# Kernel optimization log

Measured on AMD Instinct MI355X. Metric: run time of the kernel, lower is better.

The kernel has to match this reference:

```python
import math
import jax, jax.numpy as jnp
import numpy as np

NUM_HEADS = 12


def _key_blocks(x, w):
    # x: [B,S,H,D] -> overlapping key blocks [B, C, 3w, H, D], block c covers
    # original key positions [c*w - w, c*w + 2w) (zero padded at the edges).
    B, S, H, D = x.shape
    C = S // w
    x_pad = jnp.pad(x, ((0, 0), (w, w), (0, 0), (0, 0)))
    idx = (jnp.arange(C) * w)[:, None] + jnp.arange(3 * w)[None, :]  # [C,3w]
    return x_pad[:, idx]


def _band_qk(q, k, w):
    # banded_gemm_qk: scores[b,i,h,j] = q[b,i,h,:] . k[b,i+j-w,h,:], j in [0,2w]
    B, S, H, D = q.shape
    C = S // w
    kb = _key_blocks(k, w)                       # [B,C,3w,H,D]
    qb = q.reshape(B, C, w, H, D)
    s = jnp.einsum('bcxhd,bcyhd->bchxy', qb, kb)  # [B,C,H,w,3w]
    row = jnp.arange(w)[:, None]
    col = row + jnp.arange(2 * w + 1)[None, :]    # diagonal extraction
    band = s[:, :, :, row, col]                   # [B,C,H,w,2w+1]
    return band.transpose(0, 1, 3, 2, 4).reshape(B, S, H, 2 * w + 1)


def _band_pv(p, v, w):
    # banded_gemm_pv: out[b,i,h,:] = sum_j p[b,i,h,j] * v[b,i+j-w,h,:]
    B, S, H, M = p.shape
    C = S // w
    vb = _key_blocks(v, w)                        # [B,C,3w,H,D]
    pb = p.reshape(B, C, w, H, M).transpose(0, 1, 3, 2, 4)  # [B,C,H,w,2w+1]
    row = jnp.arange(w)[:, None]
    col = row + jnp.arange(2 * w + 1)[None, :]
    p_full = jnp.zeros((B, C, H, w, 3 * w), p.dtype).at[:, :, :, row, col].set(pb)
    out = jnp.einsum('bchxy,bcyhd->bcxhd', p_full, vb)  # [B,C,w,H,D]
    return out.reshape(B, S, H, -1)


def setup_inputs():
    key = jax.random.key(0)
    ks = jax.random.split(key, 14)
    B, S, E, G = 2, 4096, 768, 64
    scale = 0.02
    hs = jax.random.normal(ks[0], (B, S, E), jnp.float32)
    mask = jnp.zeros((B, 1, 1, S), jnp.int32).at[:, :, :, :G].set(1)
    def lin(k):
        kw, kb = jax.random.split(k)
        return (jax.random.normal(kw, (E, E), jnp.float32) * scale,
                jax.random.normal(kb, (E,), jnp.float32) * scale)
    Wq, bq = lin(ks[1]); Wk, bk = lin(ks[2]); Wv, bv = lin(ks[3])
    Wqg, bqg = lin(ks[4]); Wkg, bkg = lin(ks[5]); Wvg, bvg = lin(ks[6])
    return dict(hidden_states=hs, attention_mask=mask,
                Wq=Wq, bq=bq, Wk=Wk, bk=bk, Wv=Wv, bv=bv,
                Wqg=Wqg, bqg=bqg, Wkg=Wkg, bkg=bkg, Wvg=Wvg, bvg=bvg,
                window=256, num_global=G)


def reference(hidden_states, attention_mask, Wq, bq, Wk, bk, Wv, bv,
              Wqg, bqg, Wkg, bkg, Wvg, bvg, window, num_global):
    B, S, E = hidden_states.shape
    H = NUM_HEADS
    D = E // H
    w, G = window, num_global
    inv_sqrt_d = 1.0 / math.sqrt(D)

    mask2d = attention_mask.reshape(B, S)
    removed = mask2d != 0  # global (or padding) keys excluded from windowed attn

    q = (hidden_states @ Wq + bq) * inv_sqrt_d
    k = hidden_states @ Wk + bk
    v = hidden_states @ Wv + bv
    q = q.reshape(B, S, H, D)
    k = k.reshape(B, S, H, D)
    v = v.reshape(B, S, H, D)

    # --- local (banded) attention scores ---
    band = _band_qk(q, k, w)                                  # [B,S,H,2w+1]
    key_pos = jnp.arange(S)[:, None] + jnp.arange(-w, w + 1)[None, :]  # [S,2w+1]
    valid = (key_pos >= 0) & (key_pos < S)
    removed_pad = jnp.pad(removed, ((0, 0), (w, w)))
    band_removed = removed_pad[:, key_pos + w]                # [B,S,2w+1]
    keep = valid[None, :, None, :] & (~band_removed)[:, :, None, :]
    band = jnp.where(keep, band, -jnp.inf)

    # --- every-token -> global-token scores (global tokens are first G) ---
    sel = jnp.einsum('blhd,bshd->blhs', q, k[:, :G])          # [B,S,H,G]
    scores = jnp.concatenate([sel, band], axis=-1)            # [B,S,H,G+2w+1]
    probs = jax.nn.softmax(scores.astype(jnp.float32), axis=-1)

    out = jnp.einsum('blhs,bshd->blhd', probs[..., :G], v[:, :G].astype(jnp.float32))
    out = out + _band_pv(probs[..., G:], v.astype(jnp.float32), w)
    out = out.astype(hidden_states.dtype).reshape(B, S, E)

    # --- global tokens attend to everything (separate projections) ---
    hg = hidden_states[:, :G]
    qg = (hg @ Wqg + bqg).reshape(B, G, H, D)
    kg = (hidden_states @ Wkg + bkg).reshape(B, S, H, D)
    vg = (hidden_states @ Wvg + bvg).reshape(B, S, H, D)
    gs = jnp.einsum('bghd,bshd->bhgs', qg, kg) * inv_sqrt_d   # [B,H,G,S]
    gp = jax.nn.softmax(gs.astype(jnp.float32), axis=-1)
    go = jnp.einsum('bhgs,bshd->bghd', gp, vg.astype(jnp.float32)).reshape(B, G, E)
    out = out.at[:, :G].set(go.astype(out.dtype))
    return out
```

## Files before the change

### kernel.cpp

```cpp
#include <hip/hip_runtime.h>
#include <hip/hip_bf16.h>


#define BB 2
#define SS 4096
#define EE 768
#define HH 12
#define DD 64
#define WW 256
#define GG 64
#define NSPLIT 16

typedef unsigned short u16;
typedef __attribute__((ext_vector_type(4))) float f4v;
typedef __attribute__((ext_vector_type(8))) short s8v;
typedef __attribute__((ext_vector_type(4))) int i4v;
typedef __attribute__((ext_vector_type(4))) unsigned short us4v;

#define MFMA_BF16(a, b, c) __builtin_amdgcn_mfma_f32_16x16x32_bf16((a), (b), (c), 0, 0, 0)

constexpr long NSE     = (long)BB * SS * EE;
constexpr long OFF_HSB = 0;
constexpr long OFF_WT  = OFF_HSB + NSE;
constexpr long OFF_Q   = OFF_WT + 6L * EE * EE;
constexpr long OFF_K   = OFF_Q + NSE;
constexpr long OFF_V   = OFF_K + NSE;
constexpr long OFF_KG  = OFF_V + NSE;
constexpr long OFF_VG  = OFF_KG + NSE;
constexpr long OFF_QG  = OFF_VG + NSE;
constexpr long OFF_VT  = OFF_QG + (long)BB * GG * EE;
constexpr long OFF_VGT = OFF_VT + NSE;

constexpr long NQTILE = (long)BB * HH * 4;
constexpr int  NLB    = BB * HH * 63;

__device__ __forceinline__ u16 f2bf(float f) {
  unsigned u = __float_as_uint(f);
  u += 0x7fffu + ((u >> 16) & 1u);
  return (u16)(u >> 16);
}

__device__ __forceinline__ unsigned pk_bf16(float a, float b) {
  union { __hip_bfloat162 h; unsigned u; } c;
  c.h = __float22bfloat162_rn(make_float2(a, b));
  return c.u;
}

__global__ __launch_bounds__(256) void k_prep(const float* __restrict__ hs,
                                              const float* __restrict__ Wq, const float* __restrict__ Wk,
                                              const float* __restrict__ Wv, const float* __restrict__ Wkg,
                                              const float* __restrict__ Wvg, const float* __restrict__ Wqg,
                                              u16* __restrict__ ws) {
  int bid = blockIdx.x;
  if (bid < 6144) {
    long i = ((long)bid * 256 + threadIdx.x) * 4;
    f4v v = *(const f4v*)(hs + i);
    us4v o;
#pragma unroll
    for (int j = 0; j < 4; ++j) o[j] = f2bf(v[j]);
    *(us4v*)(ws + OFF_HSB + i) = o;
    return;
  }
  int wb = bid - 6144;
  int widx = wb / 576; int rem = wb % 576; int kt = rem / 24; int nt = rem % 24;
  const float* src;
  switch (widx) {
    case 0: src = Wq; break; case 1: src = Wk; break; case 2: src = Wv; break;
    case 3: src = Wkg; break; case 4: src = Wvg; break; default: src = Wqg; break;
  }
  __shared__ float tl[32][33];
  int t = threadIdx.x; int r = t >> 3; int c4 = (t & 7) * 4;
  f4v v = *(const f4v*)(src + (long)(kt * 32 + r) * EE + nt * 32 + c4);
#pragma unroll
  for (int j = 0; j < 4; ++j) tl[r][c4 + j] = v[j];
  __syncthreads();
  us4v o;
#pragma unroll
  for (int j = 0; j < 4; ++j) o[j] = f2bf(tl[c4 + j][r]);
  *(us4v*)(ws + OFF_WT + (long)widx * EE * EE + (long)(nt * 32 + r) * EE + kt * 32 + c4) = o;
}

__global__ __launch_bounds__(256, 4) void k_proj(u16* __restrict__ ws,
                                              const float* __restrict__ bq, const float* __restrict__ bk,
                                              const float* __restrict__ bv, const float* __restrict__ bkg,
                                              const float* __restrict__ bvg, const float* __restrict__ bqg) {
  int bid = blockIdx.x;
  int widx, mt, nt;
  if (bid < 1920) {
    int L = (bid & 7) * 240 + (bid >> 3);
    mt = L / 30; int inner = L % 30; widx = inner / 6; nt = inner % 6;
  } else { widx = 5; mt = 0; nt = bid - 1920; }

  __shared__ u16 Al[128 * 64];
  __shared__ u16 Bl[128 * 64];
  int tid = threadIdx.x, lane = tid & 63, wid = tid >> 6;
  int wr = wid >> 1, wc = wid & 1;

  f4v acc[4][4];
#pragma unroll
  for (int i = 0; i < 4; ++i)
#pragma unroll
    for (int j = 0; j < 4; ++j) acc[i][j] = f4v{0.f, 0.f, 0.f, 0.f};

  const u16* hsb = ws + OFF_HSB;
  const u16* Wp  = ws + OFF_WT + (long)widx * EE * EE;

  const u16* asrc[4]; const u16* bsrc[4];
  int dso[4];
#pragma unroll
  for (int it = 0; it < 4; ++it) {
    int c = tid + it * 256;
    int r = c >> 3, j = c & 7;
    long arow;
    if (widx == 5) { int rr = mt * 128 + r; arow = (long)(rr >> 6) * SS + (rr & 63); }
    else           { arow = (long)mt * 128 + r; }
    asrc[it] = hsb + arow * EE + j * 8;
    bsrc[it] = Wp + (long)(nt * 128 + r) * EE + j * 8;
    dso[it]  = r * 64 + (j ^ (r & 7)) * 8;
  }

  const u16* afp[4]; const u16* bfp[4];
#pragma unroll
  for (int f = 0; f < 4; ++f) {
    afp[f] = Al + (wr * 64 + f * 16 + (lane & 15)) * 64;
    bfp[f] = Bl + (wc * 64 + f * 16 + (lane & 15)) * 64;
  }
  int hi4 = lane >> 4, lx = lane & 7;

  i4v areg[4], breg[4];
#pragma unroll
  for (int it = 0; it < 4; ++it) {
    areg[it] = *(const i4v*)(asrc[it]);
    breg[it] = *(const i4v*)(bsrc[it]);
  }
#pragma unroll
  for (int it = 0; it < 4; ++it) {
    *(i4v*)&Al[dso[it]] = areg[it];
    *(i4v*)&Bl[dso[it]] = breg[it];
  }
  __syncthreads();

  for (int t = 0; t < 12; ++t) {
    if (t < 11) {
      int k0n = (t + 1) * 64;
#pragma unroll
      for (int it = 0; it < 4; ++it) {
        areg[it] = *(const i4v*)(asrc[it] + k0n);
        breg[it] = *(const i4v*)(bsrc[it] + k0n);
      }
    }
#pragma unroll
    for (int ks = 0; ks < 2; ++ks) {
      int sw = ((ks * 4 + hi4) ^ lx) * 8;
      s8v af[4], bfr[4];
#pragma unroll
      for (int f = 0; f < 4; ++f) {
        af[f]  = *(const s8v*)(afp[f] + sw);
        bfr[f] = *(const s8v*)(bfp[f] + sw);
      }
#pragma unroll
      for (int i = 0; i < 4; ++i)
#pragma unroll
        for (int j = 0; j < 4; ++j) acc[i][j] = MFMA_BF16(af[i], bfr[j], acc[i][j]);
    }
    __syncthreads();
    if (t < 11) {
#pragma unroll
      for (int it = 0; it < 4; ++it) {
        *(i4v*)&Al[dso[it]] = areg[it];
        *(i4v*)&Bl[dso[it]] = breg[it];
      }
    }
    __syncthreads();
  }

  const float* bias; u16* outp; float scl = 1.0f;
  switch (widx) {
    case 0: bias = bq;  outp = ws + OFF_Q;  scl = 0.125f * 1.44269504f; break;
    case 1: bias = bk;  outp = ws + OFF_K;  break;
    case 2: bias = bv;  outp = ws + OFF_VT;  break;
    case 3: bias = bkg; outp = ws + OFF_KG; break;
    case 4: bias = bvg; outp = ws + OFF_VGT; break;
    default: bias = bqg; outp = ws + OFF_QG; scl = 0.125f * 1.44269504f; break;
  }

  if (widx == 2 || widx == 4) {
    int s0g = mt * 128 + wr * 64 + (lane >> 4) * 4;
#pragma unroll
    for (int fi = 0; fi < 4; ++fi) {
      int srow = s0g + fi * 16;
      int b_ = srow >> 12; int sl = srow & (SS - 1);
#pragma unroll
      for (int fj = 0; fj < 4; ++fj) {
        int col = nt * 128 + wc * 64 + fj * 16 + (lane & 15);
        float bcol = bias[col];
        us4v o;
#pragma unroll
        for (int e = 0; e < 4; ++e) o[e] = f2bf(acc[fi][fj][e] + bcol);
        *(us4v*)&outp[((long)(b_ * HH + (col >> 6)) * DD + (col & 63)) * SS + sl] = o;
      }
    }
  } else {
#pragma unroll
    for (int fi = 0; fi < 4; ++fi)
#pragma unroll
      for (int fj = 0; fj < 4; ++fj) {
        int col = nt * 128 + wc * 64 + fj * 16 + (lane & 15);
        float bcol = bias[col];
#pragma unroll
        for (int e = 0; e < 4; ++e) {
          int rl = wr * 64 + fi * 16 + (lane >> 4) * 4 + e;
          float vv = (acc[fi][fj][e] + bcol) * scl;
          outp[(long)(mt * 128 + rl) * EE + col] = f2bf(vv);
        }
      }
  }
}

__global__ __launch_bounds__(256) void k_lattn(const u16* __restrict__ ws, float* __restrict__ out) {
  int bid0 = blockIdx.x;
  if (bid0 >= NLB) {
    int g = bid0 - NLB;
    int b = g / (HH * 4); int rem = g % (HH * 4); int h = rem >> 2; int qs = rem & 3;
    int tid = threadIdx.x;
    int row = tid >> 4; int c4 = (tid & 15) * 4;

    const float* PA = (const float*)(ws + OFF_V);
    const float* Pm = PA + NQTILE * NSPLIT * 1024L;
    const float* Pl2 = Pm + NQTILE * NSPLIT * 16L;
    long base = (long)g * NSPLIT;

    float M = -1e30f;
#pragma unroll
    for (int s = 0; s < NSPLIT; ++s) M = fmaxf(M, Pm[(base + s) * 16 + row]);
    f4v acc = f4v{0.f, 0.f, 0.f, 0.f};
    float L = 0.f;
#pragma unroll
    for (int s = 0; s < NSPLIT; ++s) {
      float wgt = exp2f(Pm[(base + s) * 16 + row] - M);
      L += wgt * Pl2[(base + s) * 16 + row];
      f4v a = *(const f4v*)&PA[(base + s) * 1024 + row * 64 + c4];
#pragma unroll
      for (int j = 0; j < 4; ++j) acc[j] += wgt * a[j];
    }
    float inv = 1.f / L;
    f4v o;
#pragma unroll
    for (int j = 0; j < 4; ++j) o[j] = acc[j] * inv;
    *(f4v*)&out[((long)b * SS + qs * 16 + row) * EE + h * DD + c4] = o;
    return;
  }

  int bid = (bid0 & 7) * 189 + (bid0 >> 3);
  int b = bid / (HH * 63); int rem = bid % (HH * 63); int h = rem / 63; int qt = rem % 63;
  int l0 = GG + qt * 64;
  int tid = threadIdx.x, lane = tid & 63, wid = tid >> 6;

  __shared__ u16 Kl[64][72];
  __shared__ u16 Vtl[64][72];
  __shared__ u16 Pl[4][16][72];

  const u16* Qp  = ws + OFF_Q + (long)b * SS * EE;
  const u16* Kp  = ws + OFF_K + (long)b * SS * EE;
  const u16* Vtp = ws + OFF_VT + (long)(b * HH + h) * DD * SS;

  int qbase = l0 + wid * 16;
  s8v qf[2];
#pragma unroll
  for (int ks = 0; ks < 2; ++ks)
    qf[ks] = *(const s8v*)(Qp + (long)(qbase + (lane & 15)) * EE + h * DD + ks * 32 + (lane >> 4) * 8);

  float m_r[4], l_p[4]; f4v ao[4];
#pragma unroll
  for (int e = 0; e < 4; ++e) { m_r[e] = -1e30f; l_p[e] = 0.f; }
#pragma unroll
  for (int df = 0; df < 4; ++df) ao[df] = f4v{0.f, 0.f, 0.f, 0.f};

  int lo = (l0 - WW > GG) ? (l0 - WW) : GG;
  int hi = (l0 + 64 + WW < SS) ? (l0 + 64 + WW) : SS;
  int ntile = 1 + ((hi - lo) >> 6);

  const u16* kbase[2]; const u16* vbase[2];
  u16* kdst[2]; u16* vdst[2];
#pragma unroll
  for (int it = 0; it < 2; ++it) {
    int c = tid + it * 256;
    int sr = c >> 3, so = (c & 7) * 8;
    kbase[it] = Kp + (long)sr * EE + h * DD + so;
    vbase[it] = Vtp + (long)sr * SS + so;
    kdst[it] = &Kl[sr][so];
    vdst[it] = &Vtl[sr][so];
  }

  i4v kreg[2], vreg[2];
#pragma unroll
  for (int it = 0; it < 2; ++it) {
    kreg[it] = *(const i4v*)(kbase[it]);
    vreg[it] = *(const i4v*)(vbase[it]);
  }
#pragma unroll
  for (int it = 0; it < 2; ++it) {
    *(i4v*)kdst[it] = kreg[it];
    *(i4v*)vdst[it] = vreg[it];
  }
  __syncthreads();

  for (int t = 0; t < ntile; ++t) {
    int kb = (t == 0) ? 0 : lo + (t - 1) * 64;
    if (t + 1 < ntile) {
      int kbn = lo + t * 64;
#pragma unroll
      for (int it = 0; it < 2; ++it) {
        kreg[it] = *(const i4v*)(kbase[it] + (long)kbn * EE);
        vreg[it] = *(const i4v*)(vbase[it] + kbn);
      }
    }

    f4v sc[4];
#pragma unroll
    for (int c = 0; c < 4; ++c) sc[c] = f4v{0.f, 0.f, 0.f, 0.f};
    __builtin_amdgcn_s_setprio(1);
#pragma unroll
    for (int c = 0; c < 4; ++c)
#pragma unroll
      for (int ks = 0; ks < 2; ++ks) {
        s8v kf = *(const s8v*)&Kl[c * 16 + (lane & 15)][ks * 32 + (lane >> 4) * 8];
        sc[c] = MFMA_BF16(qf[ks], kf, sc[c]);
      }
    __builtin_amdgcn_s_setprio(0);

    if (t > 0 && (kb <= l0 - WW || kb >= l0 + WW)) {
#pragma unroll
      for (int c = 0; c < 4; ++c) {
        int key = kb + c * 16 + (lane & 15);
#pragma unroll
        for (int e = 0; e < 4; ++e) {
          int qrow = qbase + (lane >> 4) * 4 + e;
          if (key < qrow - WW || key > qrow + WW) sc[c][e] = -1e30f;
        }
      }
    }

    float pmax[4];
#pragma unroll
    for (int e = 0; e < 4; ++e)
      pmax[e] = fmaxf(fmaxf(sc[0][e], sc[1][e]), fmaxf(sc[2][e], sc[3][e]));
    bool need;
    if (t == 0) need = true;
    else {
      bool ok = (pmax[0] <= m_r[0] + 11.5f) & (pmax[1] <= m_r[1] + 11.5f) &
                (pmax[2] <= m_r[2] + 11.5f) & (pmax[3] <= m_r[3] + 11.5f);
      need = !__all(ok);
    }
    if (need) {
#pragma unroll
      for (int e = 0; e < 4; ++e) {
        float rm = pmax[e];
#pragma unroll
        for (int off = 1; off < 16; off <<= 1) rm = fmaxf(rm, __shfl_xor(rm, off));
        float mn = fmaxf(m_r[e], rm);
        float scl = exp2f(m_r[e] - mn);
        l_p[e] *= scl;
#pragma unroll
        for (int df = 0; df < 4; ++df) ao[df][e] *= scl;
        m_r[e] = mn;
      }
    }

#pragma unroll
    for (int e = 0; e < 4; ++e) {
      float p0 = exp2f(sc[0][e] - m_r[e]);
      float p1 = exp2f(sc[1][e] - m_r[e]);
      float p2 = exp2f(sc[2][e] - m_r[e]);
      float p3 = exp2f(sc[3][e] - m_r[e]);
      l_p[e] += (p0 + p1) + (p2 + p3);
      unsigned u01 = pk_bf16(p0, p1);
      unsigned u23 = pk_bf16(p2, p3);
      int pr = (lane >> 4) * 4 + e;
      int l15 = lane & 15;
      Pl[wid][pr][l15]      = (u16)u01;
      Pl[wid][pr][16 + l15] = (u16)(u01 >> 16);
      Pl[wid][pr][32 + l15] = (u16)u23;
      Pl[wid][pr][48 + l15] = (u16)(u23 >> 16);
    }

    __builtin_amdgcn_s_setprio(1);
#pragma unroll
    for (int kblk = 0; kblk < 2; ++kblk) {
      s8v pf = *(const s8v*)&Pl[wid][lane & 15][kblk * 32 + (lane >> 4) * 8];
#pragma unroll
      for (int df = 0; df < 4; ++df) {
        s8v vf = *(const s8v*)&Vtl[df * 16 + (lane & 15)][kblk * 32 + (lane >> 4) * 8];
        ao[df] = MFMA_BF16(pf, vf, ao[df]);
      }
    }
    __builtin_amdgcn_s_setprio(0);
    __syncthreads();

    if (t + 1 < ntile) {
#pragma unroll
      for (int it = 0; it < 2; ++it) {
        *(i4v*)kdst[it] = kreg[it];
        *(i4v*)vdst[it] = vreg[it];
      }
    }
    __syncthreads();
  }

  float l_r[4];
#pragma unroll
  for (int e = 0; e < 4; ++e) {
    float s = l_p[e];
#pragma unroll
    for (int off = 1; off < 16; off <<= 1) s += __shfl_xor(s, off);
    l_r[e] = s;
  }
#pragma unroll
  for (int df = 0; df < 4; ++df)
#pragma unroll
    for (int e = 0; e < 4; ++e) {
      int row = qbase + (lane >> 4) * 4 + e;
      int col = h * DD + df * 16 + (lane & 15);
      out[((long)b * SS + row) * EE + col] = ao[df][e] / l_r[e];
    }
}

__global__ __launch_bounds__(64) void k_gattn_part(u16* __restrict__ ws) {
  int bid = blockIdx.x;
  int g = bid / NSPLIT; int sp = bid % NSPLIT;
  int b = g / (HH * 4); int rem = g % (HH * 4); int h = rem >> 2; int qs = rem & 3;
  int lane = threadIdx.x;

  __shared__ u16 Kl[32][72];
  __shared__ u16 Vtl[64][40];
  __shared__ u16 Pl[16][40];

  const u16* Qgp = ws + OFF_QG + (long)b * GG * EE;
  const u16* Kgp = ws + OFF_KG + (long)b * SS * EE;
  const u16* Vtp = ws + OFF_VGT + (long)(b * HH + h) * DD * SS;

  int qbase = qs * 16;
  s8v qf[2];
#pragma unroll
  for (int ks = 0; ks < 2; ++ks)
    qf[ks] = *(const s8v*)(Qgp + (long)(qbase + (lane & 15)) * EE + h * DD + ks * 32 + (lane >> 4) * 8);

  float m_r[4], l_p[4]; f4v ao[4];
#pragma unroll
  for (int e = 0; e < 4; ++e) { m_r[e] = -1e30f; l_p[e] = 0.f; }
#pragma unroll
  for (int df = 0; df < 4; ++df) ao[df] = f4v{0.f, 0.f, 0.f, 0.f};

  int t0 = sp * (SS / 32 / NSPLIT);
  for (int kt = t0; kt < t0 + SS / 32 / NSPLIT; ++kt) {
    int kb = kt * 32;
#pragma unroll
    for (int r2 = 0; r2 < 4; ++r2) {
      int chunk = lane + r2 * 64;
      int kr = chunk >> 3, ko = (chunk & 7) * 8;
      *(i4v*)&Kl[kr][ko] = *(const i4v*)(Kgp + (long)(kb + kr) * EE + h * DD + ko);
      int dr = chunk >> 2, ko2 = (chunk & 3) * 8;
      *(i4v*)&Vtl[dr][ko2] = *(const i4v*)(Vtp + (long)dr * SS + kb + ko2);
    }
    __syncthreads();

    f4v sc[2] = {f4v{0.f, 0.f, 0.f, 0.f}, f4v{0.f, 0.f, 0.f, 0.f}};
#pragma unroll
    for (int c = 0; c < 2; ++c)
#pragma unroll
      for (int ks = 0; ks < 2; ++ks) {
        s8v kf = *(const s8v*)&Kl[c * 16 + (lane & 15)][ks * 32 + (lane >> 4) * 8];
        sc[c] = MFMA_BF16(qf[ks], kf, sc[c]);
      }

    float pmax[4];
#pragma unroll
    for (int e = 0; e < 4; ++e) pmax[e] = fmaxf(sc[0][e], sc[1][e]);
    bool need;
    if (kt == t0) need = true;
    else {
      bool ok = (pmax[0] <= m_r[0] + 11.5f) & (pmax[1] <= m_r[1] + 11.5f) &
                (pmax[2] <= m_r[2] + 11.5f) & (pmax[3] <= m_r[3] + 11.5f);
      need = !__all(ok);
    }
    if (need) {
#pragma unroll
      for (int e = 0; e < 4; ++e) {
        float rm = pmax[e];
#pragma unroll
        for (int off = 1; off < 16; off <<= 1) rm = fmaxf(rm, __shfl_xor(rm, off));
        float mn = fmaxf(m_r[e], rm);
        float scl = exp2f(m_r[e] - mn);
        l_p[e] *= scl;
#pragma unroll
        for (int df = 0; df < 4; ++df) ao[df][e] *= scl;
        m_r[e] = mn;
      }
    }

#pragma unroll
    for (int e = 0; e < 4; ++e) {
      float p0 = exp2f(sc[0][e] - m_r[e]);
      float p1 = exp2f(sc[1][e] - m_r[e]);
      l_p[e] += p0 + p1;
      unsigned u01 = pk_bf16(p0, p1);
      int pr = (lane >> 4) * 4 + e;
      int l15 = lane & 15;
      Pl[pr][l15]      = (u16)u01;
      Pl[pr][16 + l15] = (u16)(u01 >> 16);
    }
    s8v pf = *(const s8v*)&Pl[lane & 15][(lane >> 4) * 8];
#pragma unroll
    for (int df = 0; df < 4; ++df) {
      s8v vf = *(const s8v*)&Vtl[df * 16 + (lane & 15)][(lane >> 4) * 8];
      ao[df] = MFMA_BF16(pf, vf, ao[df]);
    }
    __syncthreads();
  }

  float l_r[4];
#pragma unroll
  for (int e = 0; e < 4; ++e) {
    float s = l_p[e];
#pragma unroll
    for (int off = 1; off < 16; off <<= 1) s += __shfl_xor(s, off);
    l_r[e] = s;
  }

  float* PA = (float*)(ws + OFF_V);
  float* Pm = PA + NQTILE * NSPLIT * 1024L;
  float* Pl2 = Pm + NQTILE * NSPLIT * 16L;
  long pb = (long)g * NSPLIT + sp;
#pragma unroll
  for (int df = 0; df < 4; ++df)
#pragma unroll
    for (int e = 0; e < 4; ++e) {
      int rl = (lane >> 4) * 4 + e;
      PA[pb * 1024 + rl * 64 + df * 16 + (lane & 15)] = ao[df][e];
    }
  if ((lane & 15) == 0) {
#pragma unroll
    for (int e = 0; e < 4; ++e) {
      int rl = (lane >> 4) * 4 + e;
      Pm[pb * 16 + rl] = m_r[e];
      Pl2[pb * 16 + rl] = l_r[e];
    }
  }
}

extern "C" void kernel_launch(void* const* d_in, const int* in_sizes, int n_in,
                              void* d_out, int out_size, void* d_ws, size_t ws_size,
                              hipStream_t stream) {
  const float* hs  = (const float*)d_in[0];
  const float* Wq  = (const float*)d_in[2];  const float* bq  = (const float*)d_in[3];
  const float* Wk  = (const float*)d_in[4];  const float* bk  = (const float*)d_in[5];
  const float* Wv  = (const float*)d_in[6];  const float* bv  = (const float*)d_in[7];
  const float* Wqg = (const float*)d_in[8];  const float* bqg = (const float*)d_in[9];
  const float* Wkg = (const float*)d_in[10]; const float* bkg = (const float*)d_in[11];
  const float* Wvg = (const float*)d_in[12]; const float* bvg = (const float*)d_in[13];
  u16* ws = (u16*)d_ws;
  float* out = (float*)d_out;

  k_prep<<<6144 + 6 * 24 * 24, 256, 0, stream>>>(hs, Wq, Wk, Wv, Wkg, Wvg, Wqg, ws);
  k_proj<<<1926, 256, 0, stream>>>(ws, bq, bk, bv, bkg, bvg, bqg);
  k_gattn_part<<<(int)(NQTILE * NSPLIT), 64, 0, stream>>>(ws);
  k_lattn<<<NLB + (int)NQTILE, 256, 0, stream>>>(ws, out);
}
```

Baseline: 136.0 us.

## Keep P in registers by computing transposed scores and using 16x16x16 MFMA

The local-attention kernel now computes S^T (K as the A operand, Q as B), so each lane holds four consecutive keys for one query row. The probabilities then feed directly as the A operand of a 16x16x16 bf16 MFMA for the PV product. This removes the shared-memory round trip for P and the per-row shuffle reductions; the row max becomes a single value per lane reduced across two shuffles. In exchange it issues twice as many smaller PV MFMAs, adds shuffles to broadcast scale factors to the output layout, and keeps the old path as a fallback when the builtin is missing.

```diff
diff --git a/kernel.cpp b/kernel.cpp
--- a/kernel.cpp
+++ b/kernel.cpp
@@ -14,10 +14,18 @@
 typedef unsigned short u16;
 typedef __attribute__((ext_vector_type(4))) float f4v;
 typedef __attribute__((ext_vector_type(8))) short s8v;
+typedef __attribute__((ext_vector_type(4))) short s4v;
 typedef __attribute__((ext_vector_type(4))) int i4v;
 typedef __attribute__((ext_vector_type(4))) unsigned short us4v;
 
 #define MFMA_BF16(a, b, c) __builtin_amdgcn_mfma_f32_16x16x32_bf16((a), (b), (c), 0, 0, 0)
+
+#if __has_builtin(__builtin_amdgcn_mfma_f32_16x16x16bf16_1k)
+#define HAVE_MFMA16 1
+#define MFMA16(a, b, c) __builtin_amdgcn_mfma_f32_16x16x16bf16_1k((a), (b), (c), 0, 0, 0)
+#else
+#define HAVE_MFMA16 0
+#endif
 
 constexpr long NSE     = (long)BB * SS * EE;
 constexpr long OFF_HSB = 0;
@@ -255,10 +263,13 @@
   int b = bid / (HH * 63); int rem = bid % (HH * 63); int h = rem / 63; int qt = rem % 63;
   int l0 = GG + qt * 64;
   int tid = threadIdx.x, lane = tid & 63, wid = tid >> 6;
+  int l15 = lane & 15, hi4 = lane >> 4;
 
   __shared__ u16 Kl[64][72];
   __shared__ u16 Vtl[64][72];
+#if !HAVE_MFMA16
   __shared__ u16 Pl[4][16][72];
+#endif
 
   const u16* Qp  = ws + OFF_Q + (long)b * SS * EE;
   const u16* Kp  = ws + OFF_K + (long)b * SS * EE;
@@ -268,11 +279,9 @@
   s8v qf[2];
 #pragma unroll
   for (int ks = 0; ks < 2; ++ks)
-    qf[ks] = *(const s8v*)(Qp + (long)(qbase + (lane & 15)) * EE + h * DD + ks * 32 + (lane >> 4) * 8);
-
-  float m_r[4], l_p[4]; f4v ao[4];
-#pragma unroll
-  for (int e = 0; e < 4; ++e) { m_r[e] = -1e30f; l_p[e] = 0.f; }
+    qf[ks] = *(const s8v*)(Qp + (long)(qbase + l15) * EE + h * DD + ks * 32 + hi4 * 8);
+
+  f4v ao[4];
 #pragma unroll
   for (int df = 0; df < 4; ++df) ao[df] = f4v{0.f, 0.f, 0.f, 0.f};
 
@@ -305,6 +314,9 @@
   }
   __syncthreads();
 
+#if HAVE_MFMA16
+  float m_s = -1e30f, l_p = 0.f;
+
   for (int t = 0; t < ntile; ++t) {
     int kb = (t == 0) ? 0 : lo + (t - 1) * 64;
     if (t + 1 < ntile) {
@@ -324,7 +336,123 @@
     for (int c = 0; c < 4; ++c)
 #pragma unroll
       for (int ks = 0; ks < 2; ++ks) {
-        s8v kf = *(const s8v*)&Kl[c * 16 + (lane & 15)][ks * 32 + (lane >> 4) * 8];
+        s8v kf = *(const s8v*)&Kl[c * 16 + l15][ks * 32 + hi4 * 8];
+        sc[c] = MFMA_BF16(kf, qf[ks], sc[c]);
+      }
+    __builtin_amdgcn_s_setprio(0);
+
+    if (t > 0 && (kb <= l0 - WW || kb >= l0 + WW)) {
+      int qrow = qbase + l15;
+#pragma unroll
+      for (int c = 0; c < 4; ++c)
+#pragma unroll
+        for (int e = 0; e < 4; ++e) {
+          int key = kb + c * 16 + hi4 * 4 + e;
+          if (key < qrow - WW || key > qrow + WW) sc[c][e] = -1e30f;
+        }
+    }
+
+    float pmax = sc[0][0];
+#pragma unroll
+    for (int c = 0; c < 4; ++c)
+#pragma unroll
+      for (int e = 0; e < 4; ++e) pmax = fmaxf(pmax, sc[c][e]);
+
+    bool need = (t == 0) || !__all(pmax <= m_s + 11.5f);
+    if (need) {
+      float rm = pmax;
+      rm = fmaxf(rm, __shfl_xor(rm, 16));
+      rm = fmaxf(rm, __shfl_xor(rm, 32));
+      float mn = fmaxf(m_s, rm);
+      float scl = exp2f(m_s - mn);
+      l_p *= scl;
+      float s0 = __shfl(scl, hi4 * 4 + 0);
+      float s1 = __shfl(scl, hi4 * 4 + 1);
+      float s2 = __shfl(scl, hi4 * 4 + 2);
+      float s3 = __shfl(scl, hi4 * 4 + 3);
+#pragma unroll
+      for (int df = 0; df < 4; ++df) {
+        ao[df][0] *= s0; ao[df][1] *= s1; ao[df][2] *= s2; ao[df][3] *= s3;
+      }
+      m_s = mn;
+    }
+
+    unsigned u01[4], u23[4];
+#pragma unroll
+    for (int c = 0; c < 4; ++c) {
+      float p0 = exp2f(sc[c][0] - m_s);
+      float p1 = exp2f(sc[c][1] - m_s);
+      float p2 = exp2f(sc[c][2] - m_s);
+      float p3 = exp2f(sc[c][3] - m_s);
+      l_p += (p0 + p1) + (p2 + p3);
+      u01[c] = pk_bf16(p0, p1);
+      u23[c] = pk_bf16(p2, p3);
+    }
+
+    __builtin_amdgcn_s_setprio(1);
+#pragma unroll
+    for (int c = 0; c < 4; ++c) {
+      union { s4v v; unsigned u[2]; } pa;
+      pa.u[0] = u01[c]; pa.u[1] = u23[c];
+#pragma unroll
+      for (int df = 0; df < 4; ++df) {
+        s4v vf = *(const s4v*)&Vtl[df * 16 + l15][c * 16 + hi4 * 4];
+        ao[df] = MFMA16(pa.v, vf, ao[df]);
+      }
+    }
+    __builtin_amdgcn_s_setprio(0);
+    __syncthreads();
+
+    if (t + 1 < ntile) {
+#pragma unroll
+      for (int it = 0; it < 2; ++it) {
+        *(i4v*)kdst[it] = kreg[it];
+        *(i4v*)vdst[it] = vreg[it];
+      }
+    }
+    __syncthreads();
+  }
+
+  float l_row = l_p;
+  l_row += __shfl_xor(l_row, 16);
+  l_row += __shfl_xor(l_row, 32);
+  float lq[4];
+#pragma unroll
+  for (int e = 0; e < 4; ++e) lq[e] = __shfl(l_row, hi4 * 4 + e);
+#pragma unroll
+  for (int df = 0; df < 4; ++df)
+#pragma unroll
+    for (int e = 0; e < 4; ++e) {
+      int row = qbase + hi4 * 4 + e;
+      int col = h * DD + df * 16 + l15;
+      out[((long)b * SS + row) * EE + col] = ao[df][e] / lq[e];
+    }
+
+#else
+  float m_r[4], l_p4[4];
+#pragma unroll
+  for (int e = 0; e < 4; ++e) { m_r[e] = -1e30f; l_p4[e] = 0.f; }
+
+  for (int t = 0; t < ntile; ++t) {
+    int kb = (t == 0) ? 0 : lo + (t - 1) * 64;
+    if (t + 1 < ntile) {
+      int kbn = lo + t * 64;
+#pragma unroll
+      for (int it = 0; it < 2; ++it) {
+        kreg[it] = *(const i4v*)(kbase[it] + (long)kbn * EE);
+        vreg[it] = *(const i4v*)(vbase[it] + kbn);
+      }
+    }
+
+    f4v sc[4];
+#pragma unroll
+    for (int c = 0; c < 4; ++c) sc[c] = f4v{0.f, 0.f, 0.f, 0.f};
+    __builtin_amdgcn_s_setprio(1);
+#pragma unroll
+    for (int c = 0; c < 4; ++c)
+#pragma unroll
+      for (int ks = 0; ks < 2; ++ks) {
+        s8v kf = *(const s8v*)&Kl[c * 16 + l15][ks * 32 + hi4 * 8];
         sc[c] = MFMA_BF16(qf[ks], kf, sc[c]);
       }
     __builtin_amdgcn_s_setprio(0);
@@ -332,10 +460,10 @@
     if (t > 0 && (kb <= l0 - WW || kb >= l0 + WW)) {
 #pragma unroll
       for (int c = 0; c < 4; ++c) {
-        int key = kb + c * 16 + (lane & 15);
+        int key = kb + c * 16 + l15;
 #pragma unroll
         for (int e = 0; e < 4; ++e) {
-          int qrow = qbase + (lane >> 4) * 4 + e;
+          int qrow = qbase + hi4 * 4 + e;
           if (key < qrow - WW || key > qrow + WW) sc[c][e] = -1e30f;
         }
       }
@@ -360,7 +488,7 @@
         for (int off = 1; off < 16; off <<= 1) rm = fmaxf(rm, __shfl_xor(rm, off));
         float mn = fmaxf(m_r[e], rm);
         float scl = exp2f(m_r[e] - mn);
-        l_p[e] *= scl;
+        l_p4[e] *= scl;
 #pragma unroll
         for (int df = 0; df < 4; ++df) ao[df][e] *= scl;
         m_r[e] = mn;
@@ -373,11 +501,10 @@
       float p1 = exp2f(sc[1][e] - m_r[e]);
       float p2 = exp2f(sc[2][e] - m_r[e]);
       float p3 = exp2f(sc[3][e] - m_r[e]);
-      l_p[e] += (p0 + p1) + (p2 + p3);
+      l_p4[e] += (p0 + p1) + (p2 + p3);
       unsigned u01 = pk_bf16(p0, p1);
       unsigned u23 = pk_bf16(p2, p3);
-      int pr = (lane >> 4) * 4 + e;
-      int l15 = lane & 15;
+      int pr = hi4 * 4 + e;
       Pl[wid][pr][l15]      = (u16)u01;
       Pl[wid][pr][16 + l15] = (u16)(u01 >> 16);
       Pl[wid][pr][32 + l15] = (u16)u23;
@@ -387,10 +514,10 @@
     __builtin_amdgcn_s_setprio(1);
 #pragma unroll
     for (int kblk = 0; kblk < 2; ++kblk) {
-      s8v pf = *(const s8v*)&Pl[wid][lane & 15][kblk * 32 + (lane >> 4) * 8];
+      s8v pf = *(const s8v*)&Pl[wid][l15][kblk * 32 + hi4 * 8];
 #pragma unroll
       for (int df = 0; df < 4; ++df) {
-        s8v vf = *(const s8v*)&Vtl[df * 16 + (lane & 15)][kblk * 32 + (lane >> 4) * 8];
+        s8v vf = *(const s8v*)&Vtl[df * 16 + l15][kblk * 32 + hi4 * 8];
         ao[df] = MFMA_BF16(pf, vf, ao[df]);
       }
     }
@@ -410,7 +537,7 @@
   float l_r[4];
 #pragma unroll
   for (int e = 0; e < 4; ++e) {
-    float s = l_p[e];
+    float s = l_p4[e];
 #pragma unroll
     for (int off = 1; off < 16; off <<= 1) s += __shfl_xor(s, off);
     l_r[e] = s;
@@ -419,10 +546,11 @@
   for (int df = 0; df < 4; ++df)
 #pragma unroll
     for (int e = 0; e < 4; ++e) {
-      int row = qbase + (lane >> 4) * 4 + e;
-      int col = h * DD + df * 16 + (lane & 15);
+      int row = qbase + hi4 * 4 + e;
+      int col = h * DD + df * 16 + l15;
       out[((long)b * SS + row) * EE + col] = ao[df][e] / l_r[e];
     }
+#endif
 }
 
 __global__ __launch_bounds__(64) void k_gattn_part(u16* __restrict__ ws) {
```

New measurement: 134.1 us (median of 2 runs). No clear change (-1.4%).
